# Optimization experiments

Hardware: AMD Instinct MI355X
Metric: run time of the kernel (lower is better)

The kernel has to match this reference:

```python
import jax, jax.numpy as jnp
import numpy as np

B, C, H, W = 16, 256, 64, 64
K, HID, ITERS, EPS = 4, 512, 3, 1e-8


def _ln(x, g, b, eps=1e-5):
    m = jnp.mean(x, axis=-1, keepdims=True)
    v = jnp.mean((x - m) ** 2, axis=-1, keepdims=True)
    return (x - m) * jax.lax.rsqrt(v + eps) * g + b


def setup_inputs() -> dict:
    key = jax.random.key(0)
    ks = jax.random.split(key, 24)

    def lin(k, o, i):
        lim = np.sqrt(6.0 / (o + i)).astype(np.float32)
        return jax.random.uniform(k, (o, i), jnp.float32, -lim, lim)

    return {
        "x": jax.random.normal(ks[0], (B, C, H, W), jnp.float32),
        "noise": jax.random.normal(ks[1], (B, K, C), jnp.float32),
        "slot_mu": jax.random.normal(ks[2], (1, 1, C), jnp.float32),
        "slot_log_sigma": jnp.zeros((1, 1, C), jnp.float32),
        "ln_in_g": jnp.ones((C,)), "ln_in_b": jnp.zeros((C,)),
        "ln_sl_g": jnp.ones((C,)), "ln_sl_b": jnp.zeros((C,)),
        "ln_mlp_g": jnp.ones((C,)), "ln_mlp_b": jnp.zeros((C,)),
        "Wq": lin(ks[3], C, C), "bq": jnp.zeros((C,)),
        "Wk": lin(ks[4], C, C), "bk": jnp.zeros((C,)),
        "Wv": lin(ks[5], C, C), "bv": jnp.zeros((C,)),
        "Wu": lin(ks[6], C, 2 * C), "bu": jnp.zeros((C,)),
        "W1": lin(ks[7], HID, C), "b1": jnp.zeros((HID,)),
        "W2": lin(ks[8], C, HID), "b2": jnp.zeros((C,)),
        "We1": lin(ks[9], C // 2, C), "be1": jnp.zeros((C // 2,)),
        "We2": lin(ks[10], 1, C // 2), "be2": jnp.zeros((1,)),
    }


def reference(x, noise, slot_mu, slot_log_sigma, ln_in_g, ln_in_b, ln_sl_g, ln_sl_b,
              ln_mlp_g, ln_mlp_b, Wq, bq, Wk, bk, Wv, bv, Wu, bu, W1, b1, W2, b2,
              We1, be1, We2, be2):
    # b c h w -> b (h w) c
    xn = x.reshape(B, C, H * W).transpose(0, 2, 1)
    xn = _ln(xn, ln_in_g, ln_in_b)
    # k, v depend only on xn; hoisted out of the loop (same math)
    k = jnp.einsum('bnc,dc->bnd', xn, Wk) + bk
    v = jnp.einsum('bnc,dc->bnd', xn, Wv) + bv
    scale = C ** (-0.5)
    slots = slot_mu + jnp.exp(slot_log_sigma) * noise
    for _ in range(ITERS):
        prev = slots
        s = _ln(slots, ln_sl_g, ln_sl_b)
        q = jnp.einsum('bkc,dc->bkd', s, Wq) + bq
        attn = jax.nn.softmax(jnp.einsum('bkc,bnc->bkn', q, k) * scale, axis=1)
        w = attn / (jnp.sum(attn, axis=-1, keepdims=True) + EPS)
        updates = jnp.einsum('bkn,bnc->bkc', w, v)
        combined = jnp.concatenate([prev, updates], axis=-1)  # (B,K,2C)
        slots = jnp.einsum('bkc,dc->bkd', combined, Wu) + bu + prev
        m = _ln(slots, ln_mlp_g, ln_mlp_b)
        h = jax.nn.gelu(jnp.einsum('bkc,hc->bkh', m, W1) + b1, approximate=False)
        slots = slots + jnp.einsum('bkh,ch->bkc', h, W2) + b2
    e = jax.nn.gelu(jnp.einsum('bkc,dc->bkd', slots, We1) + be1, approximate=False)
    slot_weights = jax.nn.sigmoid(jnp.einsum('bkd,od->bko', e, We2) + be2)[..., 0]
    return slots, slot_weights
```

## Files before the change

kernel.cpp:

```cpp
#include <hip/hip_runtime.h>
#include <math.h>

#define B_    16
#define C_    256
#define NPIX  4096
#define K_    4
#define HID_  512
#define ITERS_ 3
#define NROWS (B_*NPIX)

typedef __attribute__((ext_vector_type(8))) short bf16x8;
typedef __attribute__((ext_vector_type(4))) float f32x4;

__device__ __forceinline__ float gelu_f(float x) {
    return 0.5f * x * (1.0f + erff(x * 0.70710678118654752f));
}

__device__ __forceinline__ unsigned short f2bf(float x) {
    union { float f; unsigned u; } v; v.f = x;
    unsigned r = v.u + 0x7fffu + ((v.u >> 16) & 1u);
    return (unsigned short)(r >> 16);
}
__device__ __forceinline__ float bflo(unsigned u) {
    union { unsigned u; float f; } v; v.u = u << 16; return v.f;
}
__device__ __forceinline__ float bfhi(unsigned u) {
    union { unsigned u; float f; } v; v.u = u & 0xffff0000u; return v.f;
}
__device__ __forceinline__ float4 shfl_xor4(float4 v, int m) {
    v.x = __shfl_xor(v.x, m); v.y = __shfl_xor(v.y, m);
    v.z = __shfl_xor(v.z, m); v.w = __shfl_xor(v.w, m);
    return v;
}
__device__ __forceinline__ void fma4(float4& a, const float4 w, const float4 s) {
    a.x = fmaf(w.x, s.x, a.x); a.y = fmaf(w.y, s.y, a.y);
    a.z = fmaf(w.z, s.z, a.z); a.w = fmaf(w.w, s.w, a.w);
}
__device__ __forceinline__ float hsum4(const float4 a) {
    return (a.x + a.y) + (a.z + a.w);
}

__device__ __forceinline__ void async_load16(const void* g, void* l) {
    __builtin_amdgcn_global_load_lds(
        (const __attribute__((address_space(1))) unsigned int*)g,
        (__attribute__((address_space(3))) unsigned int*)l, 16, 0, 0);
}

__device__ __forceinline__ void reduce256_in1024(float* red1, float* red2, int tid,
                                                 float& o1, float& o2) {
    __syncthreads();
    for (int s = 128; s > 0; s >>= 1) {
        if (tid < s) { red1[tid] += red1[tid + s]; red2[tid] += red2[tid + s]; }
        __syncthreads();
    }
    o1 = red1[0]; o2 = red2[0];
    __syncthreads();
}

__global__ void prep_kernel(const float* __restrict__ Wk, const float* __restrict__ Wv,
                            const float* __restrict__ Wq, const float* __restrict__ Wu,
                            const float* __restrict__ W1, const float* __restrict__ W2,
                            const float* __restrict__ We1,
                            unsigned short* __restrict__ Wtb, float4* __restrict__ Wq4,
                            float4* __restrict__ Wu4, float4* __restrict__ W14,
                            float4* __restrict__ W24, float4* __restrict__ We14) {
    int t = blockIdx.x * 256 + threadIdx.x;
    if (t < 131072) {
        int d = t >> 8, c = t & 255;
        float v = (d < 256) ? Wk[d * 256 + c] : Wv[(d - 256) * 256 + c];
        Wtb[t] = f2bf(v);
    } else {
        int i = t - 131072;
        if (i < 16384) {
            int c4 = i >> 8, d = i & 255;
            Wq4[i] = *(const float4*)&Wq[d * 256 + c4 * 4];
        } else if (i < 49152) {
            int i2 = i - 16384; int c4 = i2 >> 8, d = i2 & 255;
            Wu4[i2] = *(const float4*)&Wu[d * 512 + c4 * 4];
        } else if (i < 81920) {
            int i2 = i - 49152; int c4 = i2 >> 9, h = i2 & 511;
            W14[i2] = *(const float4*)&W1[h * 256 + c4 * 4];
        } else if (i < 114688) {
            int i2 = i - 81920; int h4 = i2 >> 8, d = i2 & 255;
            W24[i2] = *(const float4*)&W2[d * 512 + h4 * 4];
        } else {
            int i2 = i - 114688; int c4 = i2 >> 7, e = i2 & 127;
            We14[i2] = *(const float4*)&We1[e * 256 + c4 * 4];
        }
    }
}

__global__ __launch_bounds__(256) void xn_fused_kernel(
    const float* __restrict__ x, const float* __restrict__ g, const float* __restrict__ bta,
    unsigned short* __restrict__ xnb) {
    __shared__ float tile[256][65];
    __shared__ float sg[256], sb[256];
    __shared__ float red1[256], red2[256];
    __shared__ float smean[64], srstd[64];
    const int tid = threadIdx.x;
    const int nt = blockIdx.x << 6, b = blockIdx.y;

    sg[tid] = g[tid]; sb[tid] = bta[tid];
    #pragma unroll
    for (int r = 0; r < 64; ++r) {
        int idx = tid + (r << 8);
        int c_l = idx >> 6, n_l = idx & 63;
        tile[c_l][n_l] = x[(size_t)(b * C_ + c_l) * NPIX + nt + n_l];
    }
    __syncthreads();
    {
        int cq = tid >> 6, n_l = tid & 63;
        float s = 0.f, s2 = 0.f;
        #pragma unroll 8
        for (int c = cq * 64; c < cq * 64 + 64; ++c) {
            float v = tile[c][n_l];
            s += v; s2 += v * v;
        }
        red1[tid] = s; red2[tid] = s2;
    }
    __syncthreads();
    if (tid < 64) {
        float s  = red1[tid] + red1[tid + 64] + red1[tid + 128] + red1[tid + 192];
        float s2 = red2[tid] + red2[tid + 64] + red2[tid + 128] + red2[tid + 192];
        float m = s * (1.0f / C_);
        smean[tid] = m;
        srstd[tid] = rsqrtf(s2 * (1.0f / C_) - m * m + 1e-5f);
    }
    __syncthreads();
    #pragma unroll
    for (int r = 0; r < 32; ++r) {
        int idx = tid + (r << 8);
        int n_l = idx >> 7, cp = idx & 127;
        int c0 = cp << 1;
        float mn = smean[n_l], rs = srstd[n_l];
        float v0 = (tile[c0][n_l] - mn) * rs * sg[c0] + sb[c0];
        float v1 = (tile[c0 + 1][n_l] - mn) * rs * sg[c0 + 1] + sb[c0 + 1];
        ushort2 o; o.x = f2bf(v0); o.y = f2bf(v1);
        *reinterpret_cast<ushort2*>(&xnb[((size_t)(b * NPIX + nt + n_l)) * C_ + c0]) = o;
    }
}

__global__ __launch_bounds__(256) void kv_gemm_mfma(
    const unsigned short* __restrict__ xnb, const unsigned short* __restrict__ Wtb,
    const float* __restrict__ bk, const float* __restrict__ bv,
    unsigned short* __restrict__ kbuf, unsigned short* __restrict__ vbuf) {
    __shared__ __align__(16) short As[128 * 32];
    __shared__ __align__(16) short Bs[128 * 32];
    __shared__ __align__(16) unsigned short Cs[128 * 136];
    const int tid = threadIdx.x;
    const int wave = tid >> 6, lane = tid & 63;
    const int mtile = blockIdx.x << 7;
    const int ntile = blockIdx.y << 7;
    const int wr = wave >> 1, wc = wave & 1;

    f32x4 acc[4][4];
    #pragma unroll
    for (int i = 0; i < 4; ++i)
        #pragma unroll
        for (int j = 0; j < 4; ++j) acc[i][j] = (f32x4)0.f;

    const int lrow = lane & 15;
    const int lk   = (lane >> 4) << 3;

    for (int kc0 = 0; kc0 < C_; kc0 += 32) {
        #pragma unroll
        for (int j = 0; j < 2; ++j) {
            int st = (wave << 1) + j;
            int row = (st << 4) + lrow;
            async_load16(&xnb[(size_t)(mtile + row) * C_ + kc0 + lk], &As[st << 9]);
            async_load16(&Wtb[(size_t)(ntile + row) * C_ + kc0 + lk], &Bs[st << 9]);
        }
        __syncthreads();
        bf16x8 af[4], bfr[4];
        #pragma unroll
        for (int mi = 0; mi < 4; ++mi)
            af[mi] = *reinterpret_cast<const bf16x8*>(&As[(((wr << 2) + mi) << 9) + lane * 8]);
        #pragma unroll
        for (int ni = 0; ni < 4; ++ni)
            bfr[ni] = *reinterpret_cast<const bf16x8*>(&Bs[(((wc << 2) + ni) << 9) + lane * 8]);
        #pragma unroll
        for (int mi = 0; mi < 4; ++mi)
            #pragma unroll
            for (int ni = 0; ni < 4; ++ni)
                acc[mi][ni] = __builtin_amdgcn_mfma_f32_16x16x32_bf16(
                    af[mi], bfr[ni], acc[mi][ni], 0, 0, 0);
        __syncthreads();
    }

    #pragma unroll
    for (int ni = 0; ni < 4; ++ni) {
        int col_l = (wc << 6) + (ni << 4) + (lane & 15);
        int gcol = ntile + col_l;
        float bias = (gcol < 256) ? bk[gcol] : bv[gcol - 256];
        #pragma unroll
        for (int mi = 0; mi < 4; ++mi) {
            int row0 = (wr << 6) + (mi << 4) + ((lane >> 4) << 2);
            #pragma unroll
            for (int r = 0; r < 4; ++r)
                Cs[(row0 + r) * 136 + col_l] = f2bf(acc[mi][ni][r] + bias);
        }
    }
    __syncthreads();
    unsigned short* obuf = (blockIdx.y < 2) ? kbuf : vbuf;
    const int cb = (blockIdx.y & 1) << 7;
    #pragma unroll
    for (int rep = 0; rep < 8; ++rep) {
        int idx = (rep << 8) + tid;
        int row = idx >> 4;
        int ch = (idx & 15) << 3;
        uint4 dd = *reinterpret_cast<const uint4*>(&Cs[row * 136 + ch]);
        *reinterpret_cast<uint4*>(&obuf[(size_t)(mtile + row) * C_ + cb + ch]) = dd;
    }
}


__device__ __forceinline__ void ln_q_1024(float v, int tid, int d, int q, int r,
                                          const float* __restrict__ g_sl,
                                          const float* __restrict__ b_sl,
                                          const float4* __restrict__ Wq4,
                                          const float* __restrict__ bq,
                                          float* __restrict__ qbuf,
                                          float* snorm, float* pq,
                                          float* redA, float* redB) {
    if (q == 0) { redA[d] = v; redB[d] = v * v; }
    float sm, s2;
    reduce256_in1024(redA, redB, tid, sm, s2);
    if (q == 0) {
        float m = sm * (1.f / C_);
        float rs = rsqrtf(s2 * (1.f / C_) - m * m + 1e-5f);
        snorm[d] = (v - m) * rs * g_sl[d] + b_sl[d];
    }
    __syncthreads();
    const float4* sn4 = (const float4*)snorm;
    float4 a0 = {0,0,0,0}, a1 = {0,0,0,0};
    int c4b = q << 4;
    #pragma unroll
    for (int i = 0; i < 16; i += 2) {
        fma4(a0, Wq4[(c4b + i) * 256 + d], sn4[c4b + i]);
        fma4(a1, Wq4[(c4b + i + 1) * 256 + d], sn4[c4b + i + 1]);
    }
    pq[q * 256 + d] = hsum4(a0) + hsum4(a1);
    __syncthreads();
    if (q == 0)
        qbuf[r * C_ + d] = pq[d] + pq[256 + d] + pq[512 + d] + pq[768 + d] + bq[d];
}

__global__ __launch_bounds__(1024) void slot_init_q_kernel(
    const float* __restrict__ noise, const float* __restrict__ mu,
    const float* __restrict__ log_sigma,
    const float* __restrict__ g_sl, const float* __restrict__ b_sl,
    const float4* __restrict__ Wq4, const float* __restrict__ bq,
    float* __restrict__ slots, float* __restrict__ qbuf) {
    __shared__ __align__(16) float snorm[256];
    __shared__ float pq[1024];
    __shared__ float redA[256], redB[256];
    int tid = threadIdx.x;
    int d = tid & 255, q = tid >> 8;
    int r = blockIdx.x;
    float v = 0.f;
    if (q == 0) {
        v = mu[d] + expf(log_sigma[d]) * noise[r * C_ + d];
        slots[r * C_ + d] = v;
    }
    ln_q_1024(v, tid, d, q, r, g_sl, b_sl, Wq4, bq, qbuf, snorm, pq, redA, redB);
}

__device__ __forceinline__ float slot_update_body(
    int tid, int d, int q, int r, const float* __restrict__ slots,
    const float* __restrict__ partials, const float* __restrict__ asump,
    const float4* __restrict__ Wu4, const float* __restrict__ bu,
    const float* __restrict__ g_mlp, const float* __restrict__ b_mlp,
    const float4* __restrict__ W14, const float* __restrict__ b1,
    const float4* __restrict__ W24, const float* __restrict__ b2,
    float* comb, float* pq, float* mrow, float* hrow,
    float* redA, float* redB, float* s_denom) {
    int b = r >> 2, kk = r & 3;
    {
        const float* pbase = partials + (size_t)b * 65536 + kk * 256 + d;
        float u0 = 0.f, u1 = 0.f, u2 = 0.f, u3 = 0.f;
        int j0 = q << 4;
        #pragma unroll
        for (int j = 0; j < 16; j += 4) {
            u0 += pbase[(j0 + j + 0) * 1024];
            u1 += pbase[(j0 + j + 1) * 1024];
            u2 += pbase[(j0 + j + 2) * 1024];
            u3 += pbase[(j0 + j + 3) * 1024];
        }
        pq[q * 256 + d] = (u0 + u1) + (u2 + u3);
    }
    if (tid < 64) {
        float dv = asump[(b * 64 + tid) * 4 + kk];
        #pragma unroll
        for (int m = 1; m <= 32; m <<= 1) dv += __shfl_xor(dv, m);
        if (tid == 0) *s_denom = dv + 1e-8f;
    }
    float prev = 0.f;
    if (q == 0) prev = slots[r * C_ + d];
    __syncthreads();
    if (q == 0) {
        comb[d] = prev;
        comb[256 + d] = (pq[d] + pq[256 + d] + pq[512 + d] + pq[768 + d]) / *s_denom;
    }
    __syncthreads();
    const float4* cb4 = (const float4*)comb;
    {
        float4 a0 = {0,0,0,0}, a1 = {0,0,0,0}, a2 = {0,0,0,0}, a3 = {0,0,0,0};
        int c4b = q << 5;
        #pragma unroll
        for (int i = 0; i < 32; i += 4) {
            float4 w0 = Wu4[(c4b + i + 0) * 256 + d];
            float4 w1 = Wu4[(c4b + i + 1) * 256 + d];
            float4 w2 = Wu4[(c4b + i + 2) * 256 + d];
            float4 w3 = Wu4[(c4b + i + 3) * 256 + d];
            fma4(a0, w0, cb4[c4b + i + 0]); fma4(a1, w1, cb4[c4b + i + 1]);
            fma4(a2, w2, cb4[c4b + i + 2]); fma4(a3, w3, cb4[c4b + i + 3]);
        }
        pq[q * 256 + d] = (hsum4(a0) + hsum4(a1)) + (hsum4(a2) + hsum4(a3));
    }
    __syncthreads();
    float nv = 0.f;
    if (q == 0) {
        nv = pq[d] + pq[256 + d] + pq[512 + d] + pq[768 + d] + bu[d] + prev;
        redA[d] = nv; redB[d] = nv * nv;
    }
    float sm, s2;
    reduce256_in1024(redA, redB, tid, sm, s2);
    if (q == 0) {
        float m = sm * (1.f / C_);
        float rs = rsqrtf(s2 * (1.f / C_) - m * m + 1e-5f);
        mrow[d] = (nv - m) * rs * g_mlp[d] + b_mlp[d];
    }
    __syncthreads();
    const float4* m4 = (const float4*)mrow;
    {
        int j = tid & 511, h2 = tid >> 9;
        float4 a0 = {0,0,0,0}, a1 = {0,0,0,0};
        int c4b = h2 << 5;
        #pragma unroll
        for (int i = 0; i < 32; i += 2) {
            float4 w0 = W14[(c4b + i + 0) * 512 + j];
            float4 w1 = W14[(c4b + i + 1) * 512 + j];
            fma4(a0, w0, m4[c4b + i + 0]); fma4(a1, w1, m4[c4b + i + 1]);
        }
        pq[h2 * 512 + j] = hsum4(a0) + hsum4(a1);
    }
    __syncthreads();
    if (tid < 512) hrow[tid] = gelu_f(pq[tid] + pq[512 + tid] + b1[tid]);
    __syncthreads();
    const float4* h4 = (const float4*)hrow;
    {
        float4 a0 = {0,0,0,0}, a1 = {0,0,0,0}, a2 = {0,0,0,0}, a3 = {0,0,0,0};
        int h4b = q << 5;
        #pragma unroll
        for (int i = 0; i < 32; i += 4) {
            float4 w0 = W24[(h4b + i + 0) * 256 + d];
            float4 w1 = W24[(h4b + i + 1) * 256 + d];
            float4 w2 = W24[(h4b + i + 2) * 256 + d];
            float4 w3 = W24[(h4b + i + 3) * 256 + d];
            fma4(a0, w0, h4[h4b + i + 0]); fma4(a1, w1, h4[h4b + i + 1]);
            fma4(a2, w2, h4[h4b + i + 2]); fma4(a3, w3, h4[h4b + i + 3]);
        }
        pq[q * 256 + d] = (hsum4(a0) + hsum4(a1)) + (hsum4(a2) + hsum4(a3));
    }
    __syncthreads();
    float ov = 0.f;
    if (q == 0)
        ov = nv + pq[d] + pq[256 + d] + pq[512 + d] + pq[768 + d] + b2[d];
    return ov;
}

__global__ __launch_bounds__(1024) void slot_update_q_kernel(
    float* __restrict__ slots, const float* __restrict__ partials, const float* __restrict__ asump,
    const float4* __restrict__ Wu4, const float* __restrict__ bu,
    const float* __restrict__ g_mlp, const float* __restrict__ b_mlp,
    const float4* __restrict__ W14, const float* __restrict__ b1,
    const float4* __restrict__ W24, const float* __restrict__ b2,
    const float* __restrict__ g_sl, const float* __restrict__ b_sl,
    const float4* __restrict__ Wq4, const float* __restrict__ bq,
    float* __restrict__ qbuf) {
    __shared__ __align__(16) float comb[512];
    __shared__ __align__(16) float mrow[256];
    __shared__ __align__(16) float hrow[512];
    __shared__ float pq[1024];
    __shared__ float redA[256], redB[256];
    __shared__ float s_denom;
    int tid = threadIdx.x;
    int d = tid & 255, q = tid >> 8;
    int r = blockIdx.x;
    float ov = slot_update_body(tid, d, q, r, slots, partials, asump, Wu4, bu,
                                g_mlp, b_mlp, W14, b1, W24, b2,
                                comb, pq, mrow, hrow, redA, redB, &s_denom);
    if (q == 0) slots[r * C_ + d] = ov;
    __syncthreads();
    ln_q_1024(ov, tid, d, q, r, g_sl, b_sl, Wq4, bq, qbuf, mrow, pq, redA, redB);
}

__global__ __launch_bounds__(1024) void slot_update_final_kernel(
    float* __restrict__ slots, const float* __restrict__ partials, const float* __restrict__ asump,
    const float4* __restrict__ Wu4, const float* __restrict__ bu,
    const float* __restrict__ g_mlp, const float* __restrict__ b_mlp,
    const float4* __restrict__ W14, const float* __restrict__ b1,
    const float4* __restrict__ W24, const float* __restrict__ b2,
    const float4* __restrict__ We14, const float* __restrict__ be1,
    const float* __restrict__ We2, const float* __restrict__ be2,
    float* __restrict__ out) {
    __shared__ __align__(16) float comb[512];
    __shared__ __align__(16) float mrow[256];
    __shared__ __align__(16) float hrow[512];
    __shared__ float pq[1024];
    __shared__ float redA[256], redB[256];
    __shared__ float s_denom;
    __shared__ float erow[128];
    int tid = threadIdx.x;
    int d = tid & 255, q = tid >> 8;
    int r = blockIdx.x;
    float ov = slot_update_body(tid, d, q, r, slots, partials, asump, Wu4, bu,
                                g_mlp, b_mlp, W14, b1, W24, b2,
                                comb, pq, mrow, hrow, redA, redB, &s_denom);
    if (q == 0) {
        out[r * C_ + d] = ov;
        mrow[d] = ov;
    }
    __syncthreads();
    const float4* m4 = (const float4*)mrow;
    {
        int e = tid & 127, o8 = tid >> 7;
        float4 a0 = {0,0,0,0}, a1 = {0,0,0,0};
        int c4b = o8 << 3;
        #pragma unroll
        for (int i = 0; i < 8; i += 2) {
            fma4(a0, We14[(c4b + i) * 128 + e], m4[c4b + i]);
            fma4(a1, We14[(c4b + i + 1) * 128 + e], m4[c4b + i + 1]);
        }
        pq[o8 * 128 + e] = hsum4(a0) + hsum4(a1);
    }
    __syncthreads();
    if (tid < 128) {
        float s = 0.f;
        #pragma unroll
        for (int o = 0; o < 8; ++o) s += pq[o * 128 + tid];
        erow[tid] = gelu_f(s + be1[tid]);
    }
    __syncthreads();
    if (tid < 64) {
        float p = We2[tid] * erow[tid] + We2[tid + 64] * erow[tid + 64];
        #pragma unroll
        for (int m = 1; m <= 32; m <<= 1) p += __shfl_xor(p, m);
        if (tid == 0) out[B_ * K_ * C_ + r] = 1.0f / (1.0f + expf(-(p + be2[0])));
    }
}

__global__ __launch_bounds__(256) void attn_fused_kernel(
    const float* __restrict__ qbuf, const unsigned short* __restrict__ kbuf,
    const unsigned short* __restrict__ vbuf,
    float* __restrict__ partials, float* __restrict__ asump) {
    __shared__ float4 qT[264];
    __shared__ float attns[K_][64];
    __shared__ float upd_s[K_][256];
    __shared__ float asw[4][4];

    const int tid = threadIdx.x;
    const int b = blockIdx.y;
    const int chunk = blockIdx.x;
    const int n0 = chunk << 6;
    const int wave = tid >> 6, lane = tid & 63;

    {
        int c = tid;
        float4 qv;
        qv.x = qbuf[b * 1024 + c];
        qv.y = qbuf[b * 1024 + 256 + c];
        qv.z = qbuf[b * 1024 + 512 + c];
        qv.w = qbuf[b * 1024 + 768 + c];
        qT[c + (c >> 5)] = qv;
    }
    __syncthreads();

    const int cpart = tid & 7;
    const int npair = tid >> 3;
    const int c0 = cpart << 5;
    float4 acc0 = {0.f, 0.f, 0.f, 0.f}, acc1 = {0.f, 0.f, 0.f, 0.f};
    const unsigned short* kbase = kbuf + ((size_t)b * NPIX + n0 + npair * 2) * C_ + c0;
    #pragma unroll
    for (int j = 0; j < 4; ++j) {
        uint4 k0 = *reinterpret_cast<const uint4*>(kbase + j * 8);
        uint4 k1 = *reinterpret_cast<const uint4*>(kbase + C_ + j * 8);
        const unsigned kw0[4] = {k0.x, k0.y, k0.z, k0.w};
        const unsigned kw1[4] = {k1.x, k1.y, k1.z, k1.w};
        #pragma unroll
        for (int jj = 0; jj < 4; ++jj) {
            int cidx = c0 + j * 8 + jj * 2 + cpart;
            float4 qa = qT[cidx];
            float4 qb = qT[cidx + 1];
            float f00 = bflo(kw0[jj]), f01 = bfhi(kw0[jj]);
            float f10 = bflo(kw1[jj]), f11 = bfhi(kw1[jj]);
            acc0.x += f00 * qa.x + f01 * qb.x;  acc0.y += f00 * qa.y + f01 * qb.y;
            acc0.z += f00 * qa.z + f01 * qb.z;  acc0.w += f00 * qa.w + f01 * qb.w;
            acc1.x += f10 * qa.x + f11 * qb.x;  acc1.y += f10 * qa.y + f11 * qb.y;
            acc1.z += f10 * qa.z + f11 * qb.z;  acc1.w += f10 * qa.w + f11 * qb.w;
        }
    }
    #pragma unroll
    for (int m = 1; m <= 4; m <<= 1) {
        acc0 = acc0 + shfl_xor4(acc0, m);
        acc1 = acc1 + shfl_xor4(acc1, m);
    }
    float4 w0, w1;
    {
        float4 l = acc0 * 0.0625f;
        float mx = fmaxf(fmaxf(l.x, l.y), fmaxf(l.z, l.w));
        w0.x = expf(l.x - mx); w0.y = expf(l.y - mx);
        w0.z = expf(l.z - mx); w0.w = expf(l.w - mx);
        float inv = 1.0f / (w0.x + w0.y + w0.z + w0.w);
        w0 = w0 * inv;
        l = acc1 * 0.0625f;
        mx = fmaxf(fmaxf(l.x, l.y), fmaxf(l.z, l.w));
        w1.x = expf(l.x - mx); w1.y = expf(l.y - mx);
        w1.z = expf(l.z - mx); w1.w = expf(l.w - mx);
        inv = 1.0f / (w1.x + w1.y + w1.z + w1.w);
        w1 = w1 * inv;
    }
    if (cpart == 0) {
        int n_l = npair * 2;
        attns[0][n_l] = w0.x; attns[1][n_l] = w0.y; attns[2][n_l] = w0.z; attns[3][n_l] = w0.w;
        attns[0][n_l + 1] = w1.x; attns[1][n_l + 1] = w1.y;
        attns[2][n_l + 1] = w1.z; attns[3][n_l + 1] = w1.w;
    }
    float4 ws = w0 + w1;
    #pragma unroll
    for (int m = 8; m <= 32; m <<= 1) ws = ws + shfl_xor4(ws, m);
    if (lane == 0) {
        asw[wave][0] = ws.x; asw[wave][1] = ws.y; asw[wave][2] = ws.z; asw[wave][3] = ws.w;
    }
    __syncthreads();
    if (tid < 4)
        asump[(b * 64 + chunk) * 4 + tid] =
            asw[0][tid] + asw[1][tid] + asw[2][tid] + asw[3][tid];

    const int h = wave >> 1;
    const int chalf = (wave & 1) << 7;
    const int c = chalf + lane * 2;
    float a0[K_] = {0.f, 0.f, 0.f, 0.f};
    float a1[K_] = {0.f, 0.f, 0.f, 0.f};
    const unsigned short* vbase = vbuf + ((size_t)b * NPIX + n0 + h * 32) * C_ + c;
    #pragma unroll 4
    for (int nn = 0; nn < 32; ++nn) {
        unsigned vv = *reinterpret_cast<const unsigned*>(vbase + (size_t)nn * C_);
        float v0 = bflo(vv), v1 = bfhi(vv);
        int n_l = h * 32 + nn;
        float q0 = attns[0][n_l], q1 = attns[1][n_l], q2 = attns[2][n_l], q3 = attns[3][n_l];
        a0[0] = fmaf(q0, v0, a0[0]); a1[0] = fmaf(q0, v1, a1[0]);
        a0[1] = fmaf(q1, v0, a0[1]); a1[1] = fmaf(q1, v1, a1[1]);
        a0[2] = fmaf(q2, v0, a0[2]); a1[2] = fmaf(q2, v1, a1[2]);
        a0[3] = fmaf(q3, v0, a0[3]); a1[3] = fmaf(q3, v1, a1[3]);
    }
    __syncthreads();
    if (h == 0) {
        #pragma unroll
        for (int k = 0; k < K_; ++k) { upd_s[k][c] = a0[k]; upd_s[k][c + 1] = a1[k]; }
    }
    __syncthreads();
    if (h == 1) {
        #pragma unroll
        for (int k = 0; k < K_; ++k) { upd_s[k][c] += a0[k]; upd_s[k][c + 1] += a1[k]; }
    }
    __syncthreads();
    float* pb = partials + (size_t)(b * 64 + chunk) * (K_ * 256);
    #pragma unroll
    for (int k = 0; k < K_; ++k) pb[k * 256 + tid] = upd_s[k][tid];
}

extern "C" void kernel_launch(void* const* d_in, const int* in_sizes, int n_in,
                              void* d_out, int out_size, void* d_ws, size_t ws_size,
                              hipStream_t stream) {
    (void)in_sizes; (void)n_in; (void)out_size; (void)ws_size;
    const float* x        = (const float*)d_in[0];
    const float* noise    = (const float*)d_in[1];
    const float* slot_mu  = (const float*)d_in[2];
    const float* slot_ls  = (const float*)d_in[3];
    const float* ln_in_g  = (const float*)d_in[4];
    const float* ln_in_b  = (const float*)d_in[5];
    const float* ln_sl_g  = (const float*)d_in[6];
    const float* ln_sl_b  = (const float*)d_in[7];
    const float* ln_mlp_g = (const float*)d_in[8];
    const float* ln_mlp_b = (const float*)d_in[9];
    const float* Wq = (const float*)d_in[10];
    const float* bq = (const float*)d_in[11];
    const float* Wk = (const float*)d_in[12];
    const float* bk = (const float*)d_in[13];
    const float* Wv = (const float*)d_in[14];
    const float* bv = (const float*)d_in[15];
    const float* Wu = (const float*)d_in[16];
    const float* bu = (const float*)d_in[17];
    const float* W1 = (const float*)d_in[18];
    const float* b1 = (const float*)d_in[19];
    const float* W2 = (const float*)d_in[20];
    const float* b2 = (const float*)d_in[21];
    const float* We1 = (const float*)d_in[22];
    const float* be1 = (const float*)d_in[23];
    const float* We2 = (const float*)d_in[24];
    const float* be2 = (const float*)d_in[25];
    float* out = (float*)d_out;

    char* ws = (char*)d_ws;
    unsigned short* kbuf = (unsigned short*)ws;
    unsigned short* vbuf = kbuf + (size_t)NROWS * C_;
    unsigned short* xnb  = vbuf + (size_t)NROWS * C_;
    unsigned short* Wtb  = xnb + (size_t)NROWS * C_;
    float4* Wq4  = (float4*)(Wtb + 512 * C_);
    float4* Wu4  = Wq4 + 16384;
    float4* W14  = Wu4 + 32768;
    float4* W24  = W14 + 32768;
    float4* We14 = W24 + 32768;
    float* slots = (float*)(We14 + 8192);
    float* qbuf  = slots + B_ * K_ * C_;
    float* partials = qbuf + B_ * K_ * C_;
    float* asump = partials + (size_t)B_ * 64 * K_ * 256;

    prep_kernel<<<992, 256, 0, stream>>>(Wk, Wv, Wq, Wu, W1, W2, We1,
                                         Wtb, Wq4, Wu4, W14, W24, We14);
    xn_fused_kernel<<<dim3(64, 16), 256, 0, stream>>>(x, ln_in_g, ln_in_b, xnb);
    slot_init_q_kernel<<<B_ * K_, 1024, 0, stream>>>(noise, slot_mu, slot_ls,
                                                     ln_sl_g, ln_sl_b, Wq4, bq, slots, qbuf);
    kv_gemm_mfma<<<dim3(512, 4), 256, 0, stream>>>(xnb, Wtb, bk, bv, kbuf, vbuf);
    for (int it = 0; it < ITERS_; ++it) {
        attn_fused_kernel<<<dim3(64, 16), 256, 0, stream>>>(qbuf, kbuf, vbuf, partials, asump);
        if (it < ITERS_ - 1) {
            slot_update_q_kernel<<<B_ * K_, 1024, 0, stream>>>(
                slots, partials, asump, Wu4, bu, ln_mlp_g, ln_mlp_b, W14, b1, W24, b2,
                ln_sl_g, ln_sl_b, Wq4, bq, qbuf);
        } else {
            slot_update_final_kernel<<<B_ * K_, 1024, 0, stream>>>(
                slots, partials, asump, Wu4, bu, ln_mlp_g, ln_mlp_b, W14, b1, W24, b2,
                We14, be1, We2, be2, out);
        }
    }
}
```

Before: 323.7 us.

## Double K-step per barrier and alias epilogue buffer onto GEMM LDS in kv_gemm

The KV GEMM kernel now loads 64 K-elements per iteration instead of 32, which halves the number of barrier pairs in the main loop. Its LDS is packed into a single 32KB buffer, and the output staging tile now reuses the A/B tile memory, with the epilogue written out in two 64-row halves. Together these cut LDS from about 50KB to 32KB per block, which should allow more resident blocks per CU. The cost is extra barriers in the epilogue and only half the waves writing during each phase.

New measurement: 330.1 us. About the same (+2.0%).

```diff
diff --git a/kernel.cpp b/kernel.cpp
--- a/kernel.cpp
+++ b/kernel.cpp
@@ -144,9 +144,11 @@
     const unsigned short* __restrict__ xnb, const unsigned short* __restrict__ Wtb,
     const float* __restrict__ bk, const float* __restrict__ bv,
     unsigned short* __restrict__ kbuf, unsigned short* __restrict__ vbuf) {
-    __shared__ __align__(16) short As[128 * 32];
-    __shared__ __align__(16) short Bs[128 * 32];
-    __shared__ __align__(16) unsigned short Cs[128 * 136];
+    __shared__ __align__(16) char smem[32768];
+    short* As = (short*)smem;
+    short* Bs = As + 8192;
+    unsigned short* Cs = (unsigned short*)smem;
+
     const int tid = threadIdx.x;
     const int wave = tid >> 6, lane = tid & 63;
     const int mtile = blockIdx.x << 7;
@@ -159,57 +161,74 @@
         #pragma unroll
         for (int j = 0; j < 4; ++j) acc[i][j] = (f32x4)0.f;
 
-    const int lrow = lane & 15;
-    const int lk   = (lane >> 4) << 3;
-
-    for (int kc0 = 0; kc0 < C_; kc0 += 32) {
+    const int srow = lane & 15;
+    const int skq  = lane >> 4;
+
+    for (int kc0 = 0; kc0 < C_; kc0 += 64) {
         #pragma unroll
         for (int j = 0; j < 2; ++j) {
-            int st = (wave << 1) + j;
-            int row = (st << 4) + lrow;
-            async_load16(&xnb[(size_t)(mtile + row) * C_ + kc0 + lk], &As[st << 9]);
-            async_load16(&Wtb[(size_t)(ntile + row) * C_ + kc0 + lk], &Bs[st << 9]);
+            #pragma unroll
+            for (int s = 0; s < 2; ++s) {
+                int st = (wave << 1) + s;
+                int gk = kc0 + (((j << 2) + skq) << 3);
+                async_load16(&xnb[(size_t)(mtile + (st << 4) + srow) * C_ + gk],
+                             &As[(st << 10) + (j << 9)]);
+                async_load16(&Wtb[(size_t)(ntile + (st << 4) + srow) * C_ + gk],
+                             &Bs[(st << 10) + (j << 9)]);
+            }
         }
         __syncthreads();
-        bf16x8 af[4], bfr[4];
-        #pragma unroll
-        for (int mi = 0; mi < 4; ++mi)
-            af[mi] = *reinterpret_cast<const bf16x8*>(&As[(((wr << 2) + mi) << 9) + lane * 8]);
-        #pragma unroll
-        for (int ni = 0; ni < 4; ++ni)
-            bfr[ni] = *reinterpret_cast<const bf16x8*>(&Bs[(((wc << 2) + ni) << 9) + lane * 8]);
-        #pragma unroll
-        for (int mi = 0; mi < 4; ++mi)
+        #pragma unroll
+        for (int h = 0; h < 2; ++h) {
+            bf16x8 af[4], bfr[4];
+            #pragma unroll
+            for (int mi = 0; mi < 4; ++mi)
+                af[mi] = *reinterpret_cast<const bf16x8*>(
+                    &As[(((wr << 2) + mi) << 10) + (h << 9) + (lane << 3)]);
             #pragma unroll
             for (int ni = 0; ni < 4; ++ni)
-                acc[mi][ni] = __builtin_amdgcn_mfma_f32_16x16x32_bf16(
-                    af[mi], bfr[ni], acc[mi][ni], 0, 0, 0);
+                bfr[ni] = *reinterpret_cast<const bf16x8*>(
+                    &Bs[(((wc << 2) + ni) << 10) + (h << 9) + (lane << 3)]);
+            #pragma unroll
+            for (int mi = 0; mi < 4; ++mi)
+                #pragma unroll
+                for (int ni = 0; ni < 4; ++ni)
+                    acc[mi][ni] = __builtin_amdgcn_mfma_f32_16x16x32_bf16(
+                        af[mi], bfr[ni], acc[mi][ni], 0, 0, 0);
+        }
         __syncthreads();
     }
 
-    #pragma unroll
-    for (int ni = 0; ni < 4; ++ni) {
-        int col_l = (wc << 6) + (ni << 4) + (lane & 15);
-        int gcol = ntile + col_l;
-        float bias = (gcol < 256) ? bk[gcol] : bv[gcol - 256];
-        #pragma unroll
-        for (int mi = 0; mi < 4; ++mi) {
-            int row0 = (wr << 6) + (mi << 4) + ((lane >> 4) << 2);
-            #pragma unroll
-            for (int r = 0; r < 4; ++r)
-                Cs[(row0 + r) * 136 + col_l] = f2bf(acc[mi][ni][r] + bias);
-        }
-    }
-    __syncthreads();
     unsigned short* obuf = (blockIdx.y < 2) ? kbuf : vbuf;
     const int cb = (blockIdx.y & 1) << 7;
     #pragma unroll
-    for (int rep = 0; rep < 8; ++rep) {
-        int idx = (rep << 8) + tid;
-        int row = idx >> 4;
-        int ch = (idx & 15) << 3;
-        uint4 dd = *reinterpret_cast<const uint4*>(&Cs[row * 136 + ch]);
-        *reinterpret_cast<uint4*>(&obuf[(size_t)(mtile + row) * C_ + cb + ch]) = dd;
+    for (int p = 0; p < 2; ++p) {
+        if (wr == p) {
+            #pragma unroll
+            for (int ni = 0; ni < 4; ++ni) {
+                int col_l = (wc << 6) + (ni << 4) + (lane & 15);
+                int gcol = ntile + col_l;
+                float bias = (gcol < 256) ? bk[gcol] : bv[gcol - 256];
+                #pragma unroll
+                for (int mi = 0; mi < 4; ++mi) {
+                    int row0 = (mi << 4) + ((lane >> 4) << 2);
+                    #pragma unroll
+                    for (int r = 0; r < 4; ++r)
+                        Cs[(row0 + r) * 136 + col_l] = f2bf(acc[mi][ni][r] + bias);
+                }
+            }
+        }
+        __syncthreads();
+        #pragma unroll
+        for (int rep = 0; rep < 4; ++rep) {
+            int idx = (rep << 8) + tid;
+            int row = idx >> 4;
+            int ch = (idx & 15) << 3;
+            uint4 dd = *reinterpret_cast<const uint4*>(&Cs[row * 136 + ch]);
+            *reinterpret_cast<uint4*>(
+                &obuf[(size_t)(mtile + (p << 6) + row) * C_ + cb + ch]) = dd;
+        }
+        __syncthreads();
     }
 }
 
```

## Fold K and V projections into slot-side math, drop the KV GEMM

Applied to the files above, without the earlier changes.

The large per-pixel K and V projections are removed. The query is pre-multiplied by Wk (q·Wk plus a per-slot offset q·bk), so attention logits are computed directly against the normalized input xnb. The update is computed as weighted sums of xnb, then projected through Wv and bias-scaled on the small slot side. This removes the 64K×256×512 GEMM and the bf16 k/v buffer writes and reads, and the attention kernel now reads a single input tensor. In exchange it adds extra small matvecs and reductions inside the slot kernels and slightly changes the rounding path.

After: 315.2 us. -2.6%, faster.

```diff
diff --git a/kernel.cpp b/kernel.cpp
--- a/kernel.cpp
+++ b/kernel.cpp
@@ -8,6 +8,7 @@
 #define HID_  512
 #define ITERS_ 3
 #define NROWS (B_*NPIX)
+#define EPS_  1e-8f
 
 typedef __attribute__((ext_vector_type(8))) short bf16x8;
 typedef __attribute__((ext_vector_type(4))) float f32x4;
@@ -40,12 +41,6 @@
     return (a.x + a.y) + (a.z + a.w);
 }
 
-__device__ __forceinline__ void async_load16(const void* g, void* l) {
-    __builtin_amdgcn_global_load_lds(
-        (const __attribute__((address_space(1))) unsigned int*)g,
-        (__attribute__((address_space(3))) unsigned int*)l, 16, 0, 0);
-}
-
 __device__ __forceinline__ void reduce256_in1024(float* red1, float* red2, int tid,
                                                  float& o1, float& o2) {
     __syncthreads();
@@ -57,36 +52,41 @@
     __syncthreads();
 }
 
-__global__ void prep_kernel(const float* __restrict__ Wk, const float* __restrict__ Wv,
-                            const float* __restrict__ Wq, const float* __restrict__ Wu,
+__global__ void prep_kernel(const float* __restrict__ Wq, const float* __restrict__ Wu,
                             const float* __restrict__ W1, const float* __restrict__ W2,
-                            const float* __restrict__ We1,
-                            unsigned short* __restrict__ Wtb, float4* __restrict__ Wq4,
-                            float4* __restrict__ Wu4, float4* __restrict__ W14,
-                            float4* __restrict__ W24, float4* __restrict__ We14) {
-    int t = blockIdx.x * 256 + threadIdx.x;
-    if (t < 131072) {
-        int d = t >> 8, c = t & 255;
-        float v = (d < 256) ? Wk[d * 256 + c] : Wv[(d - 256) * 256 + c];
-        Wtb[t] = f2bf(v);
+                            const float* __restrict__ We1, const float* __restrict__ Wk,
+                            const float* __restrict__ Wv,
+                            float4* __restrict__ Wq4, float4* __restrict__ Wu4,
+                            float4* __restrict__ W14, float4* __restrict__ W24,
+                            float4* __restrict__ We14, float4* __restrict__ Wkq4,
+                            float4* __restrict__ Wv4) {
+    int i = blockIdx.x * 256 + threadIdx.x;
+    if (i < 16384) {
+        int c4 = i >> 8, d = i & 255;
+        Wq4[i] = *(const float4*)&Wq[d * 256 + c4 * 4];
+    } else if (i < 49152) {
+        int j = i - 16384; int c4 = j >> 8, d = j & 255;
+        Wu4[j] = *(const float4*)&Wu[d * 512 + c4 * 4];
+    } else if (i < 81920) {
+        int j = i - 49152; int c4 = j >> 9, h = j & 511;
+        W14[j] = *(const float4*)&W1[h * 256 + c4 * 4];
+    } else if (i < 114688) {
+        int j = i - 81920; int h4 = j >> 8, d = j & 255;
+        W24[j] = *(const float4*)&W2[d * 512 + h4 * 4];
+    } else if (i < 122880) {
+        int j = i - 114688; int c4 = j >> 7, e = j & 127;
+        We14[j] = *(const float4*)&We1[e * 256 + c4 * 4];
+    } else if (i < 139264) {
+        int j = i - 122880; int d4 = j >> 8, c = j & 255;
+        float4 o;
+        o.x = Wk[(4 * d4 + 0) * 256 + c];
+        o.y = Wk[(4 * d4 + 1) * 256 + c];
+        o.z = Wk[(4 * d4 + 2) * 256 + c];
+        o.w = Wk[(4 * d4 + 3) * 256 + c];
+        Wkq4[j] = o;
     } else {
-        int i = t - 131072;
-        if (i < 16384) {
-            int c4 = i >> 8, d = i & 255;
-            Wq4[i] = *(const float4*)&Wq[d * 256 + c4 * 4];
-        } else if (i < 49152) {
-            int i2 = i - 16384; int c4 = i2 >> 8, d = i2 & 255;
-            Wu4[i2] = *(const float4*)&Wu[d * 512 + c4 * 4];
-        } else if (i < 81920) {
-            int i2 = i - 49152; int c4 = i2 >> 9, h = i2 & 511;
-            W14[i2] = *(const float4*)&W1[h * 256 + c4 * 4];
-        } else if (i < 114688) {
-            int i2 = i - 81920; int h4 = i2 >> 8, d = i2 & 255;
-            W24[i2] = *(const float4*)&W2[d * 512 + h4 * 4];
-        } else {
-            int i2 = i - 114688; int c4 = i2 >> 7, e = i2 & 127;
-            We14[i2] = *(const float4*)&We1[e * 256 + c4 * 4];
-        }
+        int j = i - 139264; int e4 = j >> 8, d = j & 255;
+        Wv4[j] = *(const float4*)&Wv[d * 256 + e4 * 4];
     }
 }
 
@@ -140,88 +140,14 @@
     }
 }
 
-__global__ __launch_bounds__(256) void kv_gemm_mfma(
-    const unsigned short* __restrict__ xnb, const unsigned short* __restrict__ Wtb,
-    const float* __restrict__ bk, const float* __restrict__ bv,
-    unsigned short* __restrict__ kbuf, unsigned short* __restrict__ vbuf) {
-    __shared__ __align__(16) short As[128 * 32];
-    __shared__ __align__(16) short Bs[128 * 32];
-    __shared__ __align__(16) unsigned short Cs[128 * 136];
-    const int tid = threadIdx.x;
-    const int wave = tid >> 6, lane = tid & 63;
-    const int mtile = blockIdx.x << 7;
-    const int ntile = blockIdx.y << 7;
-    const int wr = wave >> 1, wc = wave & 1;
-
-    f32x4 acc[4][4];
-    #pragma unroll
-    for (int i = 0; i < 4; ++i)
-        #pragma unroll
-        for (int j = 0; j < 4; ++j) acc[i][j] = (f32x4)0.f;
-
-    const int lrow = lane & 15;
-    const int lk   = (lane >> 4) << 3;
-
-    for (int kc0 = 0; kc0 < C_; kc0 += 32) {
-        #pragma unroll
-        for (int j = 0; j < 2; ++j) {
-            int st = (wave << 1) + j;
-            int row = (st << 4) + lrow;
-            async_load16(&xnb[(size_t)(mtile + row) * C_ + kc0 + lk], &As[st << 9]);
-            async_load16(&Wtb[(size_t)(ntile + row) * C_ + kc0 + lk], &Bs[st << 9]);
-        }
-        __syncthreads();
-        bf16x8 af[4], bfr[4];
-        #pragma unroll
-        for (int mi = 0; mi < 4; ++mi)
-            af[mi] = *reinterpret_cast<const bf16x8*>(&As[(((wr << 2) + mi) << 9) + lane * 8]);
-        #pragma unroll
-        for (int ni = 0; ni < 4; ++ni)
-            bfr[ni] = *reinterpret_cast<const bf16x8*>(&Bs[(((wc << 2) + ni) << 9) + lane * 8]);
-        #pragma unroll
-        for (int mi = 0; mi < 4; ++mi)
-            #pragma unroll
-            for (int ni = 0; ni < 4; ++ni)
-                acc[mi][ni] = __builtin_amdgcn_mfma_f32_16x16x32_bf16(
-                    af[mi], bfr[ni], acc[mi][ni], 0, 0, 0);
-        __syncthreads();
-    }
-
-    #pragma unroll
-    for (int ni = 0; ni < 4; ++ni) {
-        int col_l = (wc << 6) + (ni << 4) + (lane & 15);
-        int gcol = ntile + col_l;
-        float bias = (gcol < 256) ? bk[gcol] : bv[gcol - 256];
-        #pragma unroll
-        for (int mi = 0; mi < 4; ++mi) {
-            int row0 = (wr << 6) + (mi << 4) + ((lane >> 4) << 2);
-            #pragma unroll
-            for (int r = 0; r < 4; ++r)
-                Cs[(row0 + r) * 136 + col_l] = f2bf(acc[mi][ni][r] + bias);
-        }
-    }
-    __syncthreads();
-    unsigned short* obuf = (blockIdx.y < 2) ? kbuf : vbuf;
-    const int cb = (blockIdx.y & 1) << 7;
-    #pragma unroll
-    for (int rep = 0; rep < 8; ++rep) {
-        int idx = (rep << 8) + tid;
-        int row = idx >> 4;
-        int ch = (idx & 15) << 3;
-        uint4 dd = *reinterpret_cast<const uint4*>(&Cs[row * 136 + ch]);
-        *reinterpret_cast<uint4*>(&obuf[(size_t)(mtile + row) * C_ + cb + ch]) = dd;
-    }
-}
-
-
-__device__ __forceinline__ void ln_q_1024(float v, int tid, int d, int q, int r,
-                                          const float* __restrict__ g_sl,
-                                          const float* __restrict__ b_sl,
-                                          const float4* __restrict__ Wq4,
-                                          const float* __restrict__ bq,
-                                          float* __restrict__ qbuf,
-                                          float* snorm, float* pq,
-                                          float* redA, float* redB) {
+
+__device__ __forceinline__ void ln_q_qt_1024(
+    float v, int tid, int d, int q, int r,
+    const float* __restrict__ g_sl, const float* __restrict__ b_sl,
+    const float4* __restrict__ Wq4, const float* __restrict__ bq,
+    const float4* __restrict__ Wkq4, const float* __restrict__ bk,
+    float* __restrict__ qtbuf, float* __restrict__ qoffbuf,
+    float* snorm, float* qrow, float* pq, float* redA, float* redB) {
     if (q == 0) { redA[d] = v; redB[d] = v * v; }
     float sm, s2;
     reduce256_in1024(redA, redB, tid, sm, s2);
@@ -231,18 +157,40 @@
         snorm[d] = (v - m) * rs * g_sl[d] + b_sl[d];
     }
     __syncthreads();
-    const float4* sn4 = (const float4*)snorm;
-    float4 a0 = {0,0,0,0}, a1 = {0,0,0,0};
-    int c4b = q << 4;
-    #pragma unroll
-    for (int i = 0; i < 16; i += 2) {
-        fma4(a0, Wq4[(c4b + i) * 256 + d], sn4[c4b + i]);
-        fma4(a1, Wq4[(c4b + i + 1) * 256 + d], sn4[c4b + i + 1]);
-    }
-    pq[q * 256 + d] = hsum4(a0) + hsum4(a1);
+    {
+        const float4* sn4 = (const float4*)snorm;
+        float4 a0 = {0,0,0,0}, a1 = {0,0,0,0};
+        int c4b = q << 4;
+        #pragma unroll
+        for (int i = 0; i < 16; i += 2) {
+            fma4(a0, Wq4[(c4b + i) * 256 + d], sn4[c4b + i]);
+            fma4(a1, Wq4[(c4b + i + 1) * 256 + d], sn4[c4b + i + 1]);
+        }
+        pq[q * 256 + d] = hsum4(a0) + hsum4(a1);
+    }
+    __syncthreads();
+    if (q == 0) {
+        float qfull = pq[d] + pq[256 + d] + pq[512 + d] + pq[768 + d] + bq[d];
+        qrow[d] = qfull;
+        redA[d] = qfull * bk[d]; redB[d] = 0.f;
+    }
+    float qoffv, dummy;
+    reduce256_in1024(redA, redB, tid, qoffv, dummy);
+    if (tid == 0) qoffbuf[r] = qoffv;
+    {
+        const float4* q4 = (const float4*)qrow;
+        float4 a0 = {0,0,0,0}, a1 = {0,0,0,0};
+        int d4b = q << 4;
+        #pragma unroll
+        for (int i = 0; i < 16; i += 2) {
+            fma4(a0, Wkq4[(d4b + i) * 256 + d], q4[d4b + i]);
+            fma4(a1, Wkq4[(d4b + i + 1) * 256 + d], q4[d4b + i + 1]);
+        }
+        pq[q * 256 + d] = hsum4(a0) + hsum4(a1);
+    }
     __syncthreads();
     if (q == 0)
-        qbuf[r * C_ + d] = pq[d] + pq[256 + d] + pq[512 + d] + pq[768 + d] + bq[d];
+        qtbuf[r * C_ + d] = pq[d] + pq[256 + d] + pq[512 + d] + pq[768 + d];
 }
 
 __global__ __launch_bounds__(1024) void slot_init_q_kernel(
@@ -250,8 +198,10 @@
     const float* __restrict__ log_sigma,
     const float* __restrict__ g_sl, const float* __restrict__ b_sl,
     const float4* __restrict__ Wq4, const float* __restrict__ bq,
-    float* __restrict__ slots, float* __restrict__ qbuf) {
+    const float4* __restrict__ Wkq4, const float* __restrict__ bk,
+    float* __restrict__ slots, float* __restrict__ qtbuf, float* __restrict__ qoffbuf) {
     __shared__ __align__(16) float snorm[256];
+    __shared__ __align__(16) float qrow[256];
     __shared__ float pq[1024];
     __shared__ float redA[256], redB[256];
     int tid = threadIdx.x;
@@ -262,18 +212,20 @@
         v = mu[d] + expf(log_sigma[d]) * noise[r * C_ + d];
         slots[r * C_ + d] = v;
     }
-    ln_q_1024(v, tid, d, q, r, g_sl, b_sl, Wq4, bq, qbuf, snorm, pq, redA, redB);
+    ln_q_qt_1024(v, tid, d, q, r, g_sl, b_sl, Wq4, bq, Wkq4, bk,
+                 qtbuf, qoffbuf, snorm, qrow, pq, redA, redB);
 }
 
 __device__ __forceinline__ float slot_update_body(
     int tid, int d, int q, int r, const float* __restrict__ slots,
     const float* __restrict__ partials, const float* __restrict__ asump,
+    const float4* __restrict__ Wv4, const float* __restrict__ bv,
     const float4* __restrict__ Wu4, const float* __restrict__ bu,
     const float* __restrict__ g_mlp, const float* __restrict__ b_mlp,
     const float4* __restrict__ W14, const float* __restrict__ b1,
     const float4* __restrict__ W24, const float* __restrict__ b2,
     float* comb, float* pq, float* mrow, float* hrow,
-    float* redA, float* redB, float* s_denom) {
+    float* redA, float* redB, float* s_denom, float* s_scale) {
     int b = r >> 2, kk = r & 3;
     {
         const float* pbase = partials + (size_t)b * 65536 + kk * 256 + d;
@@ -292,15 +244,30 @@
         float dv = asump[(b * 64 + tid) * 4 + kk];
         #pragma unroll
         for (int m = 1; m <= 32; m <<= 1) dv += __shfl_xor(dv, m);
-        if (tid == 0) *s_denom = dv + 1e-8f;
+        if (tid == 0) { *s_denom = dv + EPS_; *s_scale = dv / (dv + EPS_); }
     }
     float prev = 0.f;
     if (q == 0) prev = slots[r * C_ + d];
     __syncthreads();
     if (q == 0) {
         comb[d] = prev;
-        comb[256 + d] = (pq[d] + pq[256 + d] + pq[512 + d] + pq[768 + d]) / *s_denom;
-    }
+        mrow[d] = (pq[d] + pq[256 + d] + pq[512 + d] + pq[768 + d]) / *s_denom;
+    }
+    __syncthreads();
+    {
+        const float4* u4 = (const float4*)mrow;
+        float4 a0 = {0,0,0,0}, a1 = {0,0,0,0};
+        int e4b = q << 4;
+        #pragma unroll
+        for (int i = 0; i < 16; i += 2) {
+            fma4(a0, Wv4[(e4b + i) * 256 + d], u4[e4b + i]);
+            fma4(a1, Wv4[(e4b + i + 1) * 256 + d], u4[e4b + i + 1]);
+        }
+        pq[q * 256 + d] = hsum4(a0) + hsum4(a1);
+    }
+    __syncthreads();
+    if (q == 0)
+        comb[256 + d] = pq[d] + pq[256 + d] + pq[512 + d] + pq[768 + d] + *s_scale * bv[d];
     __syncthreads();
     const float4* cb4 = (const float4*)comb;
     {
@@ -371,32 +338,36 @@
 
 __global__ __launch_bounds__(1024) void slot_update_q_kernel(
     float* __restrict__ slots, const float* __restrict__ partials, const float* __restrict__ asump,
+    const float4* __restrict__ Wv4, const float* __restrict__ bv,
     const float4* __restrict__ Wu4, const float* __restrict__ bu,
     const float* __restrict__ g_mlp, const float* __restrict__ b_mlp,
     const float4* __restrict__ W14, const float* __restrict__ b1,
     const float4* __restrict__ W24, const float* __restrict__ b2,
     const float* __restrict__ g_sl, const float* __restrict__ b_sl,
     const float4* __restrict__ Wq4, const float* __restrict__ bq,
-    float* __restrict__ qbuf) {
+    const float4* __restrict__ Wkq4, const float* __restrict__ bk,
+    float* __restrict__ qtbuf, float* __restrict__ qoffbuf) {
     __shared__ __align__(16) float comb[512];
     __shared__ __align__(16) float mrow[256];
     __shared__ __align__(16) float hrow[512];
     __shared__ float pq[1024];
     __shared__ float redA[256], redB[256];
-    __shared__ float s_denom;
+    __shared__ float s_denom, s_scale;
     int tid = threadIdx.x;
     int d = tid & 255, q = tid >> 8;
     int r = blockIdx.x;
-    float ov = slot_update_body(tid, d, q, r, slots, partials, asump, Wu4, bu,
+    float ov = slot_update_body(tid, d, q, r, slots, partials, asump, Wv4, bv, Wu4, bu,
                                 g_mlp, b_mlp, W14, b1, W24, b2,
-                                comb, pq, mrow, hrow, redA, redB, &s_denom);
+                                comb, pq, mrow, hrow, redA, redB, &s_denom, &s_scale);
     if (q == 0) slots[r * C_ + d] = ov;
     __syncthreads();
-    ln_q_1024(ov, tid, d, q, r, g_sl, b_sl, Wq4, bq, qbuf, mrow, pq, redA, redB);
+    ln_q_qt_1024(ov, tid, d, q, r, g_sl, b_sl, Wq4, bq, Wkq4, bk,
+                 qtbuf, qoffbuf, mrow, comb, pq, redA, redB);
 }
 
 __global__ __launch_bounds__(1024) void slot_update_final_kernel(
     float* __restrict__ slots, const float* __restrict__ partials, const float* __restrict__ asump,
+    const float4* __restrict__ Wv4, const float* __restrict__ bv,
     const float4* __restrict__ Wu4, const float* __restrict__ bu,
     const float* __restrict__ g_mlp, const float* __restrict__ b_mlp,
     const float4* __restrict__ W14, const float* __restrict__ b1,
@@ -409,14 +380,14 @@
     __shared__ __align__(16) float hrow[512];
     __shared__ float pq[1024];
     __shared__ float redA[256], redB[256];
-    __shared__ float s_denom;
+    __shared__ float s_denom, s_scale;
     __shared__ float erow[128];
     int tid = threadIdx.x;
     int d = tid & 255, q = tid >> 8;
     int r = blockIdx.x;
-    float ov = slot_update_body(tid, d, q, r, slots, partials, asump, Wu4, bu,
+    float ov = slot_update_body(tid, d, q, r, slots, partials, asump, Wv4, bv, Wu4, bu,
                                 g_mlp, b_mlp, W14, b1, W24, b2,
-                                comb, pq, mrow, hrow, redA, redB, &s_denom);
+                                comb, pq, mrow, hrow, redA, redB, &s_denom, &s_scale);
     if (q == 0) {
         out[r * C_ + d] = ov;
         mrow[d] = ov;
@@ -451,13 +422,14 @@
 }
 
 __global__ __launch_bounds__(256) void attn_fused_kernel(
-    const float* __restrict__ qbuf, const unsigned short* __restrict__ kbuf,
-    const unsigned short* __restrict__ vbuf,
+    const float* __restrict__ qtbuf, const float* __restrict__ qoffbuf,
+    const unsigned short* __restrict__ xnb,
     float* __restrict__ partials, float* __restrict__ asump) {
     __shared__ float4 qT[264];
     __shared__ float attns[K_][64];
     __shared__ float upd_s[K_][256];
     __shared__ float asw[4][4];
+    __shared__ float4 qo_s;
 
     const int tid = threadIdx.x;
     const int b = blockIdx.y;
@@ -468,11 +440,12 @@
     {
         int c = tid;
         float4 qv;
-        qv.x = qbuf[b * 1024 + c];
-        qv.y = qbuf[b * 1024 + 256 + c];
-        qv.z = qbuf[b * 1024 + 512 + c];
-        qv.w = qbuf[b * 1024 + 768 + c];
+        qv.x = qtbuf[b * 1024 + c];
+        qv.y = qtbuf[b * 1024 + 256 + c];
+        qv.z = qtbuf[b * 1024 + 512 + c];
+        qv.w = qtbuf[b * 1024 + 768 + c];
         qT[c + (c >> 5)] = qv;
+        if (tid == 0) qo_s = *(const float4*)&qoffbuf[b * 4];
     }
     __syncthreads();
 
@@ -480,7 +453,7 @@
     const int npair = tid >> 3;
     const int c0 = cpart << 5;
     float4 acc0 = {0.f, 0.f, 0.f, 0.f}, acc1 = {0.f, 0.f, 0.f, 0.f};
-    const unsigned short* kbase = kbuf + ((size_t)b * NPIX + n0 + npair * 2) * C_ + c0;
+    const unsigned short* kbase = xnb + ((size_t)b * NPIX + n0 + npair * 2) * C_ + c0;
     #pragma unroll
     for (int j = 0; j < 4; ++j) {
         uint4 k0 = *reinterpret_cast<const uint4*>(kbase + j * 8);
@@ -507,13 +480,13 @@
     }
     float4 w0, w1;
     {
-        float4 l = acc0 * 0.0625f;
+        float4 l = (acc0 + qo_s) * 0.0625f;
         float mx = fmaxf(fmaxf(l.x, l.y), fmaxf(l.z, l.w));
         w0.x = expf(l.x - mx); w0.y = expf(l.y - mx);
         w0.z = expf(l.z - mx); w0.w = expf(l.w - mx);
         float inv = 1.0f / (w0.x + w0.y + w0.z + w0.w);
         w0 = w0 * inv;
-        l = acc1 * 0.0625f;
+        l = (acc1 + qo_s) * 0.0625f;
         mx = fmaxf(fmaxf(l.x, l.y), fmaxf(l.z, l.w));
         w1.x = expf(l.x - mx); w1.y = expf(l.y - mx);
         w1.z = expf(l.z - mx); w1.w = expf(l.w - mx);
@@ -542,7 +515,7 @@
     const int c = chalf + lane * 2;
     float a0[K_] = {0.f, 0.f, 0.f, 0.f};
     float a1[K_] = {0.f, 0.f, 0.f, 0.f};
-    const unsigned short* vbase = vbuf + ((size_t)b * NPIX + n0 + h * 32) * C_ + c;
+    const unsigned short* vbase = xnb + ((size_t)b * NPIX + n0 + h * 32) * C_ + c;
     #pragma unroll 4
     for (int nn = 0; nn < 32; ++nn) {
         unsigned vv = *reinterpret_cast<const unsigned*>(vbase + (size_t)nn * C_);
@@ -603,36 +576,37 @@
     float* out = (float*)d_out;
 
     char* ws = (char*)d_ws;
-    unsigned short* kbuf = (unsigned short*)ws;
-    unsigned short* vbuf = kbuf + (size_t)NROWS * C_;
-    unsigned short* xnb  = vbuf + (size_t)NROWS * C_;
-    unsigned short* Wtb  = xnb + (size_t)NROWS * C_;
-    float4* Wq4  = (float4*)(Wtb + 512 * C_);
+    unsigned short* xnb = (unsigned short*)ws;
+    float4* Wq4  = (float4*)(xnb + (size_t)NROWS * C_);
     float4* Wu4  = Wq4 + 16384;
     float4* W14  = Wu4 + 32768;
     float4* W24  = W14 + 32768;
     float4* We14 = W24 + 32768;
-    float* slots = (float*)(We14 + 8192);
-    float* qbuf  = slots + B_ * K_ * C_;
-    float* partials = qbuf + B_ * K_ * C_;
+    float4* Wkq4 = We14 + 8192;
+    float4* Wv4  = Wkq4 + 16384;
+    float* slots = (float*)(Wv4 + 16384);
+    float* qtbuf = slots + B_ * K_ * C_;
+    float* qoffb = qtbuf + B_ * K_ * C_;
+    float* partials = qoffb + B_ * K_;
     float* asump = partials + (size_t)B_ * 64 * K_ * 256;
 
-    prep_kernel<<<992, 256, 0, stream>>>(Wk, Wv, Wq, Wu, W1, W2, We1,
-                                         Wtb, Wq4, Wu4, W14, W24, We14);
+    prep_kernel<<<608, 256, 0, stream>>>(Wq, Wu, W1, W2, We1, Wk, Wv,
+                                         Wq4, Wu4, W14, W24, We14, Wkq4, Wv4);
     xn_fused_kernel<<<dim3(64, 16), 256, 0, stream>>>(x, ln_in_g, ln_in_b, xnb);
     slot_init_q_kernel<<<B_ * K_, 1024, 0, stream>>>(noise, slot_mu, slot_ls,
-                                                     ln_sl_g, ln_sl_b, Wq4, bq, slots, qbuf);
-    kv_gemm_mfma<<<dim3(512, 4), 256, 0, stream>>>(xnb, Wtb, bk, bv, kbuf, vbuf);
+                                                     ln_sl_g, ln_sl_b, Wq4, bq, Wkq4, bk,
+                                                     slots, qtbuf, qoffb);
     for (int it = 0; it < ITERS_; ++it) {
-        attn_fused_kernel<<<dim3(64, 16), 256, 0, stream>>>(qbuf, kbuf, vbuf, partials, asump);
+        attn_fused_kernel<<<dim3(64, 16), 256, 0, stream>>>(qtbuf, qoffb, xnb,
+                                                            partials, asump);
         if (it < ITERS_ - 1) {
             slot_update_q_kernel<<<B_ * K_, 1024, 0, stream>>>(
-                slots, partials, asump, Wu4, bu, ln_mlp_g, ln_mlp_b, W14, b1, W24, b2,
-                ln_sl_g, ln_sl_b, Wq4, bq, qbuf);
+                slots, partials, asump, Wv4, bv, Wu4, bu, ln_mlp_g, ln_mlp_b,
+                W14, b1, W24, b2, ln_sl_g, ln_sl_b, Wq4, bq, Wkq4, bk, qtbuf, qoffb);
         } else {
             slot_update_final_kernel<<<B_ * K_, 1024, 0, stream>>>(
-                slots, partials, asump, Wu4, bu, ln_mlp_g, ln_mlp_b, W14, b1, W24, b2,
-                We14, be1, We2, be2, out);
-        }
-    }
-}
+                slots, partials, asump, Wv4, bv, Wu4, bu, ln_mlp_g, ln_mlp_b,
+                W14, b1, W24, b2, We14, be1, We2, be2, out);
+        }
+    }
+}
```
